# Kernel optimization log

Measured on AMD Instinct MI355X. Metric: run time of the kernel, lower is better.

Reference implementation:

```python
import jax, jax.numpy as jnp
import numpy as np

N = 50000   # num gloss nodes
H = 768     # gnn_hidden_size (BERT-base hidden)
NEG = 0.2   # GATv2 leaky_relu negative_slope
EPS = 1e-5  # LayerNorm eps


def ln_gelu(x, g, b):
    # LayerNorm -> exact GELU (torch GELU default); Dropout is identity in eval
    mu = x.mean(-1, keepdims=True)
    var = ((x - mu) ** 2).mean(-1, keepdims=True)
    x = (x - mu) / jnp.sqrt(var + EPS) * g + b
    return jax.nn.gelu(x, approximate=False)


def gatv2(x, src, dst, Wl, bl, Wr, br, att, bias):
    # PyG GATv2Conv, heads=1: e_ij = a^T LeakyReLU(Wl x_j + Wr x_i), softmax over incoming edges
    xl = x @ Wl + bl              # source transform [N,H]
    xr = x @ Wr + br              # target transform [N,H]
    e = jax.nn.leaky_relu(xl[src] + xr[dst], NEG) @ att   # [E]
    m = jax.ops.segment_max(e, dst, num_segments=N)
    a = jnp.exp(e - m[dst])
    denom = jax.ops.segment_sum(a, dst, num_segments=N)
    alpha = a / denom[dst]
    out = jax.ops.segment_sum(alpha[:, None] * xl[src], dst, num_segments=N)
    return out + bias


def setup_inputs() -> dict:
    key = jax.random.key(0)
    ks = jax.random.split(key, 20)
    d = {
        "input_embeddings": jax.random.normal(ks[0], (32, H), dtype=jnp.float32),
        "node_feats": jax.random.normal(ks[1], (N, H), dtype=jnp.float32),
        "edges": jax.random.randint(ks[2], (2, 100000), 0, N, dtype=jnp.int64)
                 if jax.config.jax_enable_x64 else
                 jax.random.randint(ks[2], (2, 100000), 0, N, dtype=jnp.int32),
        "labels_size": 4096,
    }
    s = 0.02
    for i, name in enumerate(["gat2", "gat3"]):
        k = ks[3 + 6 * i: 9 + 6 * i]
        d[name + "_Wl"] = jax.random.normal(k[0], (H, H), dtype=jnp.float32) * s
        d[name + "_bl"] = jnp.zeros((H,), jnp.float32)
        d[name + "_Wr"] = jax.random.normal(k[1], (H, H), dtype=jnp.float32) * s
        d[name + "_br"] = jnp.zeros((H,), jnp.float32)
        d[name + "_att"] = jax.random.normal(k[2], (H,), dtype=jnp.float32) * s
        d[name + "_bias"] = jnp.zeros((H,), jnp.float32)
    for i in (1, 2, 3):
        d[f"ln{i}_g"] = jnp.ones((H,), jnp.float32)
        d[f"ln{i}_b"] = jnp.zeros((H,), jnp.float32)
    return d


def reference(input_embeddings, node_feats, edges, labels_size,
              gat2_Wl, gat2_bl, gat2_Wr, gat2_br, gat2_att, gat2_bias,
              gat3_Wl, gat3_bl, gat3_Wr, gat3_br, gat3_att, gat3_bias,
              ln1_g, ln1_b, ln2_g, ln2_b, ln3_g, ln3_b):
    loops = jnp.arange(N, dtype=edges.dtype)           # add_self_loops=True
    src = jnp.concatenate([edges[0], loops])
    dst = jnp.concatenate([edges[1], loops])
    x = ln_gelu(node_feats, ln1_g, ln1_b)
    x = gatv2(x, src, dst, gat2_Wl, gat2_bl, gat2_Wr, gat2_br, gat2_att, gat2_bias)
    x = ln_gelu(x, ln2_g, ln2_b)
    x = gatv2(x, src, dst, gat3_Wl, gat3_bl, gat3_Wr, gat3_br, gat3_att, gat3_bias)
    x = ln_gelu(x, ln3_g, ln3_b)
    gnn_vector = x[:labels_size]
    return (input_embeddings, gnn_vector)
```

## Files before the change

kernel.cpp:

```cpp
#include <hip/hip_runtime.h>
#include <hip/hip_bf16.h>
#include <math.h>

#define H 768
#define BM 128

typedef __attribute__((ext_vector_type(4))) float f32x4;
typedef __attribute__((ext_vector_type(8))) short bf16x8;

__device__ __forceinline__ float bf2f(unsigned u16v){
  return __uint_as_float((u16v & 0xffffu) << 16);
}
__device__ __forceinline__ unsigned f2bf2(float a, float b){
  __hip_bfloat16 ha = __float2bfloat16(a), hb = __float2bfloat16(b);
  return (unsigned)*(unsigned short*)&ha | ((unsigned)*(unsigned short*)&hb << 16);
}
__device__ __forceinline__ float gelu_exact(float x){
  return 0.5f * x * (1.0f + erff(x * 0.70710678118654752f));
}
__device__ __forceinline__ void gload16(const void* g, void* l){
  __builtin_amdgcn_global_load_lds(
      (const __attribute__((address_space(1))) unsigned int*)g,
      (__attribute__((address_space(3))) unsigned int*)l,
      16, 0, 0);
}
__device__ __forceinline__ float wave_sum(float p){
#pragma unroll
  for (int o = 32; o; o >>= 1) p += __shfl_xor(p, o);
  return p;
}

__global__ __launch_bounds__(256) void lnw_list_kernel(
    const float* __restrict__ in, const float* __restrict__ g,
    const float* __restrict__ b, __hip_bfloat16* __restrict__ out,
    const int* __restrict__ rlist, const int* __restrict__ np){
  int i = blockIdx.x * 4 + (threadIdx.x >> 6);
  if (i >= *np) return;
  int row = rlist[i];
  int lane = threadIdx.x & 63;
  const float* rp = in + (size_t)row * H;
  float v[12];
#pragma unroll
  for (int q = 0; q < 3; q++){
    float4 t = *(const float4*)&rp[(lane + q * 64) * 4];
    v[q*4+0] = t.x; v[q*4+1] = t.y; v[q*4+2] = t.z; v[q*4+3] = t.w;
  }
  float s = 0.f;
#pragma unroll
  for (int t = 0; t < 12; t++) s += v[t];
  float mean = wave_sum(s) * (1.0f / H);
  float s2 = 0.f;
#pragma unroll
  for (int t = 0; t < 12; t++){ float d = v[t] - mean; s2 += d * d; }
  float rstd = rsqrtf(wave_sum(s2) * (1.0f / H) + 1e-5f);
  unsigned* op = (unsigned*)(out + (size_t)row * H);
#pragma unroll
  for (int q = 0; q < 3; q++){
    float4 gv = *(const float4*)&g[(lane + q * 64) * 4];
    float4 bv = *(const float4*)&b[(lane + q * 64) * 4];
    float z0 = gelu_exact((v[q*4+0] - mean) * rstd * gv.x + bv.x);
    float z1 = gelu_exact((v[q*4+1] - mean) * rstd * gv.y + bv.y);
    float z2 = gelu_exact((v[q*4+2] - mean) * rstd * gv.z + bv.z);
    float z3 = gelu_exact((v[q*4+3] - mean) * rstd * gv.w + bv.w);
    uint2 pk; pk.x = f2bf2(z0, z1); pk.y = f2bf2(z2, z3);
    *(uint2*)&op[lane * 2 + q * 128] = pk;
  }
}

__global__ __launch_bounds__(256) void wt_bf16_kernel(
    const float* __restrict__ W0, const float* __restrict__ W1,
    const float* __restrict__ W2, const float* __restrict__ W3,
    __hip_bfloat16* __restrict__ T0, __hip_bfloat16* __restrict__ T1,
    __hip_bfloat16* __restrict__ T2, __hip_bfloat16* __restrict__ T3){
  int z = blockIdx.z;
  const float* W = (z == 0) ? W0 : (z == 1) ? W1 : (z == 2) ? W2 : W3;
  __hip_bfloat16* WT = (z == 0) ? T0 : (z == 1) ? T1 : (z == 2) ? T2 : T3;
  __shared__ float tile[32][33];
  int k0 = blockIdx.x * 32, n0 = blockIdx.y * 32;
  int tx = threadIdx.x & 31, ty = threadIdx.x >> 5;
#pragma unroll
  for (int i = 0; i < 32; i += 8)
    tile[ty + i][tx] = W[(size_t)(k0 + ty + i) * H + n0 + tx];
  __syncthreads();
#pragma unroll
  for (int i = 0; i < 32; i += 8)
    WT[(size_t)(n0 + ty + i) * H + k0 + tx] = __float2bfloat16(tile[tx][ty + i]);
}

__global__ __launch_bounds__(256, 3) void gemm_fused_kernel(
    const __hip_bfloat16* __restrict__ A,
    const __hip_bfloat16* __restrict__ WT,
    const float* __restrict__ bl, const float* __restrict__ br,
    __hip_bfloat16* __restrict__ Cl, __hip_bfloat16* __restrict__ Cr,
    const int* __restrict__ rmapL, const int* __restrict__ nrLp,
    const int* __restrict__ rmapR, const int* __restrict__ nrRp, int MrR){
  __shared__ char smem[49152];

  int wgid = blockIdx.x;
  int panel = wgid / 12, colblk = wgid % 12;
  int row0 = panel * BM;
  const bool is_r = colblk >= 6;
  const int* rmap = is_r ? rmapR : rmapL;
  int nr = is_r ? (rmapR ? *nrRp : MrR) : *nrLp;
  if (row0 >= nr) return;
  const bool remap = (rmap != nullptr);

  const int t = threadIdx.x;
  const int sr = t >> 2;
  const int scs = (((t & 3) ^ ((sr >> 1) & 3)) * 8);
  const int t16 = t * 16;
  int ra0 = min(row0 + sr, nr - 1), ra1 = min(row0 + sr + 64, nr - 1);
  if (remap){ ra0 = rmap[ra0]; ra1 = rmap[ra1]; }
  const __hip_bfloat16* pa0 = A + (size_t)ra0 * H + scs;
  const __hip_bfloat16* pa1 = A + (size_t)ra1 * H + scs;
  const __hip_bfloat16* pb0 = WT + (size_t)(colblk * 128 + sr) * H + scs;
  const __hip_bfloat16* pb1 = pb0 + (size_t)64 * H;

  const int l = t & 63, w = t >> 6;
  const int wm = (w >> 1) * 64, wn = (w & 1) * 64;
  const int r0 = l & 15;
  const int kcs2 = (((l >> 4) ^ ((r0 >> 1) & 3)) * 16);

  f32x4 acc[4][4];
#pragma unroll
  for (int m = 0; m < 4; m++)
#pragma unroll
    for (int n = 0; n < 4; n++) acc[m][n] = (f32x4){0.f, 0.f, 0.f, 0.f};

#define STAGE(kt, b) do{                                   \
    int _k0 = (kt) * 32;                                   \
    char* _bs = smem + (b) * 16384;                        \
    gload16(pa0 + _k0, _bs + t16);                         \
    gload16(pa1 + _k0, _bs + 4096 + t16);                  \
    gload16(pb0 + _k0, _bs + 8192 + t16);                  \
    gload16(pb1 + _k0, _bs + 12288 + t16);                 \
  }while(0)

  STAGE(0, 0);
  STAGE(1, 1);

  for (int kt = 0; kt < 24; kt++){
    if (kt < 23) asm volatile("s_waitcnt vmcnt(4)" ::: "memory");
    else         asm volatile("s_waitcnt vmcnt(0)" ::: "memory");
    __builtin_amdgcn_s_barrier();
    __builtin_amdgcn_sched_barrier(0);
    if (kt + 2 < 24) STAGE(kt + 2, (kt + 2) % 3);
    const char* base = smem + (kt % 3) * 16384;
    bf16x8 af[4], bfr[4];
#pragma unroll
    for (int m = 0; m < 4; m++)
      af[m]  = *(const bf16x8*)(base + (wm + m * 16 + r0) * 64 + kcs2);
#pragma unroll
    for (int n = 0; n < 4; n++)
      bfr[n] = *(const bf16x8*)(base + 8192 + (wn + n * 16 + r0) * 64 + kcs2);
#pragma unroll
    for (int m = 0; m < 4; m++)
#pragma unroll
      for (int n = 0; n < 4; n++)
        acc[m][n] = __builtin_amdgcn_mfma_f32_16x16x32_bf16(af[m], bfr[n], acc[m][n], 0, 0, 0);
  }
#undef STAGE

  __syncthreads();
  const int rgrp = (l >> 4) * 4;
  const float* bp = is_r ? br : bl;
  const int cb = (is_r ? colblk - 6 : colblk) * 128;
#pragma unroll
  for (int n = 0; n < 4; n++){
    int lc = wn + n * 16 + r0;
    float bb = bp[cb + lc];
#pragma unroll
    for (int m = 0; m < 4; m++){
#pragma unroll
      for (int jj = 0; jj < 4; jj++){
        int lr = wm + m * 16 + rgrp + jj;
        int byte = lr * 256 + ((lc * 2) ^ (((lr >> 2) & 3) << 5));
        *(__hip_bfloat16*)(smem + byte) = __float2bfloat16(acc[m][n][jj] + bb);
      }
    }
  }
  __syncthreads();
  __hip_bfloat16* C = is_r ? Cr : Cl;
#pragma unroll
  for (int p = 0; p < 8; p++){
    int ba = p * 4096 + t16;
    int lr = ba >> 8, inner = ba & 255;
    int gr = row0 + lr;
    if (gr >= nr) continue;
    int orow = remap ? rmap[gr] : gr;
    uint4 v = *(const uint4*)(smem + lr * 256 + (inner ^ (((lr >> 2) & 3) << 5)));
    *(uint4*)(C + (size_t)orow * H + cb + (inner >> 1)) = v;
  }
}

__device__ __forceinline__ int e_src(const int* ep, int E0, int k){
  return (k < E0) ? ep[k] : (k - E0);
}
__device__ __forceinline__ int e_dst(const int* ep, int E0, int k){
  return (k < E0) ? ep[E0 + k] : (k - E0);
}

__global__ __launch_bounds__(256) void count_mark_kernel(const int* __restrict__ ep,
                                                         int E0, int E, int L,
                                                         int* __restrict__ cnt,
                                                         int* __restrict__ flag){
  int k = blockIdx.x * 256 + threadIdx.x;
  if (k >= E) return;
  int d = e_dst(ep, E0, k);
  atomicAdd(&cnt[d], 1);
  if (d < L) flag[e_src(ep, E0, k)] = 1;
}

__global__ __launch_bounds__(256) void mark2_kernel(const int* __restrict__ ep,
                                                    int E0, int E,
                                                    const int* __restrict__ flag,
                                                    int* __restrict__ flag2){
  int k = blockIdx.x * 256 + threadIdx.x;
  if (k >= E) return;
  if (flag[e_dst(ep, E0, k)]) flag2[e_src(ep, E0, k)] = 1;
}

__global__ __launch_bounds__(1024) void scan1_tri_kernel(
    const int* __restrict__ a0, int* __restrict__ o0, int* __restrict__ s0,
    const int* __restrict__ a1, int* __restrict__ o1, int* __restrict__ s1,
    const int* __restrict__ a2, int* __restrict__ o2, int* __restrict__ s2, int n){
  __shared__ int lds[1024];
  const int* as[3] = {a0, a1, a2};
  int* os[3] = {o0, o1, o2};
  int* ss[3] = {s0, s1, s2};
  int tid = threadIdx.x;
  int gi = blockIdx.x * 1024 + tid;
  for (int q = 0; q < 3; q++){
    __syncthreads();
    int v = (gi < n) ? as[q][gi] : 0;
    lds[tid] = v;
    __syncthreads();
    for (int o = 1; o < 1024; o <<= 1){
      int tv = (tid >= o) ? lds[tid - o] : 0;
      __syncthreads();
      lds[tid] += tv;
      __syncthreads();
    }
    if (gi < n) os[q][gi] = lds[tid] - v;
    if (tid == 1023) ss[q][blockIdx.x] = lds[1023];
  }
}

__global__ void scan2_tri_kernel(int* __restrict__ s0, int* __restrict__ o0,
                                 int* __restrict__ s1, int* __restrict__ o1,
                                 int* __restrict__ s2, int* __restrict__ o2,
                                 int nb, int n){
  int lane = threadIdx.x;
  int* ss[3] = {s0, s1, s2};
  int* os[3] = {o0, o1, o2};
  for (int q = 0; q < 3; q++){
    int v = (lane < nb) ? ss[q][lane] : 0;
    int incl = v;
#pragma unroll
    for (int o = 1; o < 64; o <<= 1){
      int t = __shfl_up(incl, o);
      if (lane >= o) incl += t;
    }
    if (lane < nb) ss[q][lane] = incl - v;
    if (lane == nb - 1) os[q][n] = incl;
  }
}

__global__ __launch_bounds__(1024) void scan3_tri_kernel(
    int* __restrict__ off, int* __restrict__ cur, const int* __restrict__ sums,
    int* __restrict__ fpos, const int* __restrict__ fsums,
    const int* __restrict__ flag, int* __restrict__ list,
    int* __restrict__ fpos2, const int* __restrict__ fsums2,
    const int* __restrict__ flag2, int* __restrict__ list2, int n){
  int gi = blockIdx.x * 1024 + threadIdx.x;
  if (gi < n){
    int v = off[gi] + sums[blockIdx.x];
    off[gi] = v;
    cur[gi] = v;
    int fp = fpos[gi] + fsums[blockIdx.x];
    fpos[gi] = fp;
    if (flag[gi]) list[fp] = gi;
    int fp2 = fpos2[gi] + fsums2[blockIdx.x];
    fpos2[gi] = fp2;
    if (flag2[gi]) list2[fp2] = gi;
  }
}

__global__ __launch_bounds__(256) void fill_kernel(const int* __restrict__ ep, int E0, int E,
                                                   int* __restrict__ cur, int* __restrict__ csr){
  int k = blockIdx.x * 256 + threadIdx.x;
  if (k >= E) return;
  int d = e_dst(ep, E0, k);
  int pos = atomicAdd(&cur[d], 1);
  csr[pos] = k;
}

template<typename OutT>
__global__ __launch_bounds__(256) void agat_kernel(
    const __hip_bfloat16* __restrict__ xl, const __hip_bfloat16* __restrict__ xr,
    const float* __restrict__ att, const int* __restrict__ off,
    const int* __restrict__ csr, const int* __restrict__ ep, int E0,
    const float* __restrict__ bias, const float* __restrict__ g,
    const float* __restrict__ b, OutT* __restrict__ out,
    const int* __restrict__ dlist, const int* __restrict__ ndp, int ndst){
  int i = blockIdx.x * 4 + (threadIdx.x >> 6);
  int lim = dlist ? *ndp : ndst;
  if (i >= lim) return;
  int d = dlist ? dlist[i] : i;
  int lane = threadIdx.x & 63;
  float xrv[12], attv[12];
  const unsigned* pr = (const unsigned*)(xr + (size_t)d * H);
#pragma unroll
  for (int q = 0; q < 3; q++){
    uint2 vr = *(const uint2*)&pr[lane * 2 + q * 128];
    float4 av = *(const float4*)&att[(lane + q * 64) * 4];
    xrv[q*4+0] = bf2f(vr.x); xrv[q*4+1] = bf2f(vr.x >> 16);
    xrv[q*4+2] = bf2f(vr.y); xrv[q*4+3] = bf2f(vr.y >> 16);
    attv[q*4+0] = av.x; attv[q*4+1] = av.y; attv[q*4+2] = av.z; attv[q*4+3] = av.w;
  }
  float m = -INFINITY, den = 0.f, acc[12];
#pragma unroll
  for (int t = 0; t < 12; t++) acc[t] = 0.f;
  int j0 = off[d], j1 = off[d + 1];
  int sj = (j0 < j1) ? e_src(ep, E0, csr[j0]) : 0;
  for (int j = j0; j < j1; j++){
    int s_ = sj;
    if (j + 1 < j1) sj = e_src(ep, E0, csr[j + 1]);
    const unsigned* pl = (const unsigned*)(xl + (size_t)s_ * H);
    float xv[12];
#pragma unroll
    for (int q = 0; q < 3; q++){
      uint2 vl = *(const uint2*)&pl[lane * 2 + q * 128];
      xv[q*4+0] = bf2f(vl.x); xv[q*4+1] = bf2f(vl.x >> 16);
      xv[q*4+2] = bf2f(vl.y); xv[q*4+3] = bf2f(vl.y >> 16);
    }
    float p = 0.f;
#pragma unroll
    for (int t = 0; t < 12; t++){
      float v = xv[t] + xrv[t];
      v = (v > 0.f) ? v : 0.2f * v;
      p += v * attv[t];
    }
    p = wave_sum(p);
    float mn = fmaxf(m, p);
    float sc = __expf(m - mn), wgt = __expf(p - mn);
    den = den * sc + wgt;
#pragma unroll
    for (int t = 0; t < 12; t++) acc[t] = acc[t] * sc + wgt * xv[t];
    m = mn;
  }
  float inv = 1.0f / den;
  float y[12];
  float s1 = 0.f;
#pragma unroll
  for (int q = 0; q < 3; q++){
    float4 bv = *(const float4*)&bias[(lane + q * 64) * 4];
    y[q*4+0] = acc[q*4+0] * inv + bv.x;
    y[q*4+1] = acc[q*4+1] * inv + bv.y;
    y[q*4+2] = acc[q*4+2] * inv + bv.z;
    y[q*4+3] = acc[q*4+3] * inv + bv.w;
  }
#pragma unroll
  for (int t = 0; t < 12; t++) s1 += y[t];
  float mean = wave_sum(s1) * (1.0f / H);
  float s2 = 0.f;
#pragma unroll
  for (int t = 0; t < 12; t++){ float dt = y[t] - mean; s2 += dt * dt; }
  float rstd = rsqrtf(wave_sum(s2) * (1.0f / H) + 1e-5f);
  OutT* op = out + (size_t)d * H;
#pragma unroll
  for (int q = 0; q < 3; q++){
    float4 gv = *(const float4*)&g[(lane + q * 64) * 4];
    float4 bv = *(const float4*)&b[(lane + q * 64) * 4];
    float z0 = gelu_exact((y[q*4+0] - mean) * rstd * gv.x + bv.x);
    float z1 = gelu_exact((y[q*4+1] - mean) * rstd * gv.y + bv.y);
    float z2 = gelu_exact((y[q*4+2] - mean) * rstd * gv.z + bv.z);
    float z3 = gelu_exact((y[q*4+3] - mean) * rstd * gv.w + bv.w);
    if constexpr (sizeof(OutT) == 2){
      uint2 pk; pk.x = f2bf2(z0, z1); pk.y = f2bf2(z2, z3);
      *(uint2*)((unsigned*)op + lane * 2 + q * 128) = pk;
    } else {
      float4 fv; fv.x = z0; fv.y = z1; fv.z = z2; fv.w = z3;
      *(float4*)&op[(lane + q * 64) * 4] = fv;
    }
  }
}

extern "C" void kernel_launch(void* const* d_in, const int* in_sizes, int n_in,
                              void* d_out, int out_size, void* d_ws, size_t ws_size,
                              hipStream_t stream){
  const float* emb   = (const float*)d_in[0];
  const float* feats = (const float*)d_in[1];
  const int*   edges = (const int*)d_in[2];
  const float* Wl2 = (const float*)d_in[4],  *bl2 = (const float*)d_in[5];
  const float* Wr2 = (const float*)d_in[6],  *br2 = (const float*)d_in[7];
  const float* att2= (const float*)d_in[8],  *bias2=(const float*)d_in[9];
  const float* Wl3 = (const float*)d_in[10], *bl3 = (const float*)d_in[11];
  const float* Wr3 = (const float*)d_in[12], *br3 = (const float*)d_in[13];
  const float* att3= (const float*)d_in[14], *bias3=(const float*)d_in[15];
  const float* g1 = (const float*)d_in[16], *b1 = (const float*)d_in[17];
  const float* g2 = (const float*)d_in[18], *b2 = (const float*)d_in[19];
  const float* g3 = (const float*)d_in[20], *b3 = (const float*)d_in[21];

  const int N  = in_sizes[1] / H;
  const int E0 = in_sizes[2] / 2;
  const int E  = E0 + N;
  const int L  = 4096;
  const int Mpad = ((N + 127) / 128) * 128;
  const int panels128 = Mpad / BM;
  const int nchunk = (N + 1023) / 1024;

  __hip_bfloat16* ab  = (__hip_bfloat16*)d_ws;
  __hip_bfloat16* xl  = ab + (size_t)Mpad * H;
  __hip_bfloat16* xr  = xl + (size_t)Mpad * H;
  __hip_bfloat16* wt2 = xr + (size_t)Mpad * H;
  __hip_bfloat16* wt3 = wt2 + (size_t)2 * H * H;
  int* cnt   = (int*)(wt3 + (size_t)2 * H * H);
  int* flag  = cnt + N;
  int* flag2 = flag + N;
  int* off   = flag2 + N;
  int* cur   = off + N + 1;
  int* csr   = cur + N;
  int* sums  = csr + E;
  int* fpos  = sums + 64;
  int* fsums = fpos + N + 1;
  int* fpos2 = fsums + 64;
  int* fsums2= fpos2 + N + 1;
  int* list  = fsums2 + 64;
  int* list2 = list + N;

  float* out_f = (float*)d_out;

  hipMemcpyAsync(out_f, emb, (size_t)in_sizes[0] * sizeof(float),
                 hipMemcpyDeviceToDevice, stream);

  hipMemsetAsync(cnt, 0, (size_t)3 * N * sizeof(int), stream);
  count_mark_kernel<<<(E + 255) / 256, 256, 0, stream>>>(edges, E0, E, L, cnt, flag);
  mark2_kernel<<<(E + 255) / 256, 256, 0, stream>>>(edges, E0, E, flag, flag2);
  scan1_tri_kernel<<<nchunk, 1024, 0, stream>>>(cnt, off, sums, flag, fpos, fsums,
                                                flag2, fpos2, fsums2, N);
  scan2_tri_kernel<<<1, 64, 0, stream>>>(sums, off, fsums, fpos, fsums2, fpos2, nchunk, N);
  scan3_tri_kernel<<<nchunk, 1024, 0, stream>>>(off, cur, sums, fpos, fsums, flag, list,
                                                fpos2, fsums2, flag2, list2, N);
  fill_kernel<<<(E + 255) / 256, 256, 0, stream>>>(edges, E0, E, cur, csr);

  dim3 wgrid(H / 32, H / 32, 4);
  wt_bf16_kernel<<<wgrid, 256, 0, stream>>>(Wl2, Wr2, Wl3, Wr3,
                                            wt2, wt2 + (size_t)H * H,
                                            wt3, wt3 + (size_t)H * H);

  const int* nS3 = fpos + N;
  const int* nS2 = fpos2 + N;

  lnw_list_kernel<<<(N + 3) / 4, 256, 0, stream>>>(feats, g1, b1, ab, list2, nS2);
  gemm_fused_kernel<<<panels128 * 12, 256, 0, stream>>>(ab, wt2, bl2, br2, xl, xr,
                                                        list2, nS2, list, nS3, 0);
  agat_kernel<__hip_bfloat16><<<(N + 3) / 4, 256, 0, stream>>>(
      xl, xr, att2, off, csr, edges, E0, bias2, g2, b2, ab, list, nS3, 0);

  gemm_fused_kernel<<<panels128 * 12, 256, 0, stream>>>(ab, wt3, bl3, br3, xl, xr,
                                                        list, nS3, nullptr, nullptr, L);
  agat_kernel<float><<<(L + 3) / 4, 256, 0, stream>>>(
      xl, xr, att3, off, csr, edges, E0, bias3, g3, b3, out_f + in_sizes[0],
      nullptr, nullptr, L);
}
```

Baseline: 206.4 us.

## Fuse graph preprocessing into one cooperative kernel and persist row kernels

Replaces the memset, count/mark, mark2, three scan kernels and the CSR fill with a single cooperative kernel that uses grid-wide syncs between phases. This removes several launches and inter-kernel gaps. The CSR fill now only writes edges whose destination is flagged, which skips work for nodes no later layer reads. The LayerNorm and aggregation kernels become grid-stride loops over a fixed grid of 2048 blocks instead of one wave per row. The cooperative launch needs all 128 blocks of 1024 threads to be co-resident, and a heavy phase such as the atomics-based count now runs on far fewer threads than before.

```diff
diff --git a/kernel.cpp b/kernel.cpp
--- a/kernel.cpp
+++ b/kernel.cpp
@@ -1,6 +1,9 @@
 #include <hip/hip_runtime.h>
+#include <hip/hip_cooperative_groups.h>
 #include <hip/hip_bf16.h>
 #include <math.h>
+
+namespace cg = cooperative_groups;
 
 #define H 768
 #define BM 128
@@ -29,41 +32,129 @@
   for (int o = 32; o; o >>= 1) p += __shfl_xor(p, o);
   return p;
 }
+__device__ __forceinline__ int e_src(const int* ep, int E0, int k){
+  return (k < E0) ? ep[k] : (k - E0);
+}
+__device__ __forceinline__ int e_dst(const int* ep, int E0, int k){
+  return (k < E0) ? ep[E0 + k] : (k - E0);
+}
+
+__global__ __launch_bounds__(1024) void preproc_kernel(
+    const int* __restrict__ ep, int E0, int E, int N, int L,
+    int* cnt, int* flag, int* flag2, int* off, int* cur, int* csr,
+    int* sums, int* fpos, int* fsums, int* fpos2, int* fsums2,
+    int* list, int* list2){
+  cg::grid_group grid = cg::this_grid();
+  __shared__ int lds[1024];
+  const int tid = threadIdx.x;
+  const int gid = blockIdx.x * blockDim.x + tid;
+  const int gsz = gridDim.x * blockDim.x;
+  const int nchunk = (N + 1023) >> 10;
+
+  for (int i = gid; i < 3 * N; i += gsz) cnt[i] = 0;
+  grid.sync();
+  for (int k = gid; k < E; k += gsz){
+    int d = e_dst(ep, E0, k);
+    atomicAdd(&cnt[d], 1);
+    if (d < L) flag[e_src(ep, E0, k)] = 1;
+  }
+  grid.sync();
+  for (int k = gid; k < E; k += gsz)
+    if (flag[e_dst(ep, E0, k)]) flag2[e_src(ep, E0, k)] = 1;
+  grid.sync();
+  {
+    const int* as[3] = {cnt, flag, flag2};
+    int* os[3] = {off, fpos, fpos2};
+    int* ss[3] = {sums, fsums, fsums2};
+    if ((int)blockIdx.x < nchunk){
+      int gi = blockIdx.x * 1024 + tid;
+      for (int q = 0; q < 3; q++){
+        __syncthreads();
+        int v = (gi < N) ? as[q][gi] : 0;
+        lds[tid] = v;
+        __syncthreads();
+        for (int o = 1; o < 1024; o <<= 1){
+          int tv = (tid >= o) ? lds[tid - o] : 0;
+          __syncthreads();
+          lds[tid] += tv;
+          __syncthreads();
+        }
+        if (gi < N) os[q][gi] = lds[tid] - v;
+        if (tid == 1023) ss[q][blockIdx.x] = lds[1023];
+      }
+    }
+  }
+  grid.sync();
+  if (blockIdx.x == 0 && tid < 64){
+    int* ss[3] = {sums, fsums, fsums2};
+    int* os[3] = {off, fpos, fpos2};
+    for (int q = 0; q < 3; q++){
+      int v = (tid < nchunk) ? ss[q][tid] : 0;
+      int incl = v;
+#pragma unroll
+      for (int o = 1; o < 64; o <<= 1){
+        int t2 = __shfl_up(incl, o);
+        if (tid >= o) incl += t2;
+      }
+      if (tid < nchunk) ss[q][tid] = incl - v;
+      if (tid == nchunk - 1) os[q][N] = incl;
+    }
+  }
+  grid.sync();
+  if ((int)blockIdx.x < nchunk){
+    int gi = blockIdx.x * 1024 + tid;
+    if (gi < N){
+      int v = off[gi] + sums[blockIdx.x];
+      off[gi] = v;
+      cur[gi] = v;
+      int fp = fpos[gi] + fsums[blockIdx.x];
+      if (flag[gi]) list[fp] = gi;
+      int fp2 = fpos2[gi] + fsums2[blockIdx.x];
+      if (flag2[gi]) list2[fp2] = gi;
+    }
+  }
+  grid.sync();
+  for (int k = gid; k < E; k += gsz){
+    int d = e_dst(ep, E0, k);
+    if (flag[d]) csr[atomicAdd(&cur[d], 1)] = k;
+  }
+}
 
 __global__ __launch_bounds__(256) void lnw_list_kernel(
     const float* __restrict__ in, const float* __restrict__ g,
     const float* __restrict__ b, __hip_bfloat16* __restrict__ out,
     const int* __restrict__ rlist, const int* __restrict__ np){
-  int i = blockIdx.x * 4 + (threadIdx.x >> 6);
-  if (i >= *np) return;
-  int row = rlist[i];
+  int lim = *np;
   int lane = threadIdx.x & 63;
-  const float* rp = in + (size_t)row * H;
-  float v[12];
-#pragma unroll
-  for (int q = 0; q < 3; q++){
-    float4 t = *(const float4*)&rp[(lane + q * 64) * 4];
-    v[q*4+0] = t.x; v[q*4+1] = t.y; v[q*4+2] = t.z; v[q*4+3] = t.w;
-  }
-  float s = 0.f;
-#pragma unroll
-  for (int t = 0; t < 12; t++) s += v[t];
-  float mean = wave_sum(s) * (1.0f / H);
-  float s2 = 0.f;
-#pragma unroll
-  for (int t = 0; t < 12; t++){ float d = v[t] - mean; s2 += d * d; }
-  float rstd = rsqrtf(wave_sum(s2) * (1.0f / H) + 1e-5f);
-  unsigned* op = (unsigned*)(out + (size_t)row * H);
-#pragma unroll
-  for (int q = 0; q < 3; q++){
-    float4 gv = *(const float4*)&g[(lane + q * 64) * 4];
-    float4 bv = *(const float4*)&b[(lane + q * 64) * 4];
-    float z0 = gelu_exact((v[q*4+0] - mean) * rstd * gv.x + bv.x);
-    float z1 = gelu_exact((v[q*4+1] - mean) * rstd * gv.y + bv.y);
-    float z2 = gelu_exact((v[q*4+2] - mean) * rstd * gv.z + bv.z);
-    float z3 = gelu_exact((v[q*4+3] - mean) * rstd * gv.w + bv.w);
-    uint2 pk; pk.x = f2bf2(z0, z1); pk.y = f2bf2(z2, z3);
-    *(uint2*)&op[lane * 2 + q * 128] = pk;
+  for (int i = blockIdx.x * 4 + (threadIdx.x >> 6); i < lim; i += gridDim.x * 4){
+    int row = rlist[i];
+    const float* rp = in + (size_t)row * H;
+    float v[12];
+#pragma unroll
+    for (int q = 0; q < 3; q++){
+      float4 t = *(const float4*)&rp[(lane + q * 64) * 4];
+      v[q*4+0] = t.x; v[q*4+1] = t.y; v[q*4+2] = t.z; v[q*4+3] = t.w;
+    }
+    float s = 0.f;
+#pragma unroll
+    for (int t = 0; t < 12; t++) s += v[t];
+    float mean = wave_sum(s) * (1.0f / H);
+    float s2 = 0.f;
+#pragma unroll
+    for (int t = 0; t < 12; t++){ float d = v[t] - mean; s2 += d * d; }
+    float rstd = rsqrtf(wave_sum(s2) * (1.0f / H) + 1e-5f);
+    unsigned* op = (unsigned*)(out + (size_t)row * H);
+#pragma unroll
+    for (int q = 0; q < 3; q++){
+      float4 gv = *(const float4*)&g[(lane + q * 64) * 4];
+      float4 bv = *(const float4*)&b[(lane + q * 64) * 4];
+      float z0 = gelu_exact((v[q*4+0] - mean) * rstd * gv.x + bv.x);
+      float z1 = gelu_exact((v[q*4+1] - mean) * rstd * gv.y + bv.y);
+      float z2 = gelu_exact((v[q*4+2] - mean) * rstd * gv.z + bv.z);
+      float z3 = gelu_exact((v[q*4+3] - mean) * rstd * gv.w + bv.w);
+      uint2 pk; pk.x = f2bf2(z0, z1); pk.y = f2bf2(z2, z3);
+      *(uint2*)&op[lane * 2 + q * 128] = pk;
+    }
   }
 }
 
@@ -193,108 +284,6 @@
   }
 }
 
-__device__ __forceinline__ int e_src(const int* ep, int E0, int k){
-  return (k < E0) ? ep[k] : (k - E0);
-}
-__device__ __forceinline__ int e_dst(const int* ep, int E0, int k){
-  return (k < E0) ? ep[E0 + k] : (k - E0);
-}
-
-__global__ __launch_bounds__(256) void count_mark_kernel(const int* __restrict__ ep,
-                                                         int E0, int E, int L,
-                                                         int* __restrict__ cnt,
-                                                         int* __restrict__ flag){
-  int k = blockIdx.x * 256 + threadIdx.x;
-  if (k >= E) return;
-  int d = e_dst(ep, E0, k);
-  atomicAdd(&cnt[d], 1);
-  if (d < L) flag[e_src(ep, E0, k)] = 1;
-}
-
-__global__ __launch_bounds__(256) void mark2_kernel(const int* __restrict__ ep,
-                                                    int E0, int E,
-                                                    const int* __restrict__ flag,
-                                                    int* __restrict__ flag2){
-  int k = blockIdx.x * 256 + threadIdx.x;
-  if (k >= E) return;
-  if (flag[e_dst(ep, E0, k)]) flag2[e_src(ep, E0, k)] = 1;
-}
-
-__global__ __launch_bounds__(1024) void scan1_tri_kernel(
-    const int* __restrict__ a0, int* __restrict__ o0, int* __restrict__ s0,
-    const int* __restrict__ a1, int* __restrict__ o1, int* __restrict__ s1,
-    const int* __restrict__ a2, int* __restrict__ o2, int* __restrict__ s2, int n){
-  __shared__ int lds[1024];
-  const int* as[3] = {a0, a1, a2};
-  int* os[3] = {o0, o1, o2};
-  int* ss[3] = {s0, s1, s2};
-  int tid = threadIdx.x;
-  int gi = blockIdx.x * 1024 + tid;
-  for (int q = 0; q < 3; q++){
-    __syncthreads();
-    int v = (gi < n) ? as[q][gi] : 0;
-    lds[tid] = v;
-    __syncthreads();
-    for (int o = 1; o < 1024; o <<= 1){
-      int tv = (tid >= o) ? lds[tid - o] : 0;
-      __syncthreads();
-      lds[tid] += tv;
-      __syncthreads();
-    }
-    if (gi < n) os[q][gi] = lds[tid] - v;
-    if (tid == 1023) ss[q][blockIdx.x] = lds[1023];
-  }
-}
-
-__global__ void scan2_tri_kernel(int* __restrict__ s0, int* __restrict__ o0,
-                                 int* __restrict__ s1, int* __restrict__ o1,
-                                 int* __restrict__ s2, int* __restrict__ o2,
-                                 int nb, int n){
-  int lane = threadIdx.x;
-  int* ss[3] = {s0, s1, s2};
-  int* os[3] = {o0, o1, o2};
-  for (int q = 0; q < 3; q++){
-    int v = (lane < nb) ? ss[q][lane] : 0;
-    int incl = v;
-#pragma unroll
-    for (int o = 1; o < 64; o <<= 1){
-      int t = __shfl_up(incl, o);
-      if (lane >= o) incl += t;
-    }
-    if (lane < nb) ss[q][lane] = incl - v;
-    if (lane == nb - 1) os[q][n] = incl;
-  }
-}
-
-__global__ __launch_bounds__(1024) void scan3_tri_kernel(
-    int* __restrict__ off, int* __restrict__ cur, const int* __restrict__ sums,
-    int* __restrict__ fpos, const int* __restrict__ fsums,
-    const int* __restrict__ flag, int* __restrict__ list,
-    int* __restrict__ fpos2, const int* __restrict__ fsums2,
-    const int* __restrict__ flag2, int* __restrict__ list2, int n){
-  int gi = blockIdx.x * 1024 + threadIdx.x;
-  if (gi < n){
-    int v = off[gi] + sums[blockIdx.x];
-    off[gi] = v;
-    cur[gi] = v;
-    int fp = fpos[gi] + fsums[blockIdx.x];
-    fpos[gi] = fp;
-    if (flag[gi]) list[fp] = gi;
-    int fp2 = fpos2[gi] + fsums2[blockIdx.x];
-    fpos2[gi] = fp2;
-    if (flag2[gi]) list2[fp2] = gi;
-  }
-}
-
-__global__ __launch_bounds__(256) void fill_kernel(const int* __restrict__ ep, int E0, int E,
-                                                   int* __restrict__ cur, int* __restrict__ csr){
-  int k = blockIdx.x * 256 + threadIdx.x;
-  if (k >= E) return;
-  int d = e_dst(ep, E0, k);
-  int pos = atomicAdd(&cur[d], 1);
-  csr[pos] = k;
-}
-
 template<typename OutT>
 __global__ __launch_bounds__(256) void agat_kernel(
     const __hip_bfloat16* __restrict__ xl, const __hip_bfloat16* __restrict__ xr,
@@ -303,85 +292,85 @@
     const float* __restrict__ bias, const float* __restrict__ g,
     const float* __restrict__ b, OutT* __restrict__ out,
     const int* __restrict__ dlist, const int* __restrict__ ndp, int ndst){
-  int i = blockIdx.x * 4 + (threadIdx.x >> 6);
   int lim = dlist ? *ndp : ndst;
-  if (i >= lim) return;
-  int d = dlist ? dlist[i] : i;
   int lane = threadIdx.x & 63;
-  float xrv[12], attv[12];
-  const unsigned* pr = (const unsigned*)(xr + (size_t)d * H);
-#pragma unroll
-  for (int q = 0; q < 3; q++){
-    uint2 vr = *(const uint2*)&pr[lane * 2 + q * 128];
-    float4 av = *(const float4*)&att[(lane + q * 64) * 4];
-    xrv[q*4+0] = bf2f(vr.x); xrv[q*4+1] = bf2f(vr.x >> 16);
-    xrv[q*4+2] = bf2f(vr.y); xrv[q*4+3] = bf2f(vr.y >> 16);
-    attv[q*4+0] = av.x; attv[q*4+1] = av.y; attv[q*4+2] = av.z; attv[q*4+3] = av.w;
-  }
-  float m = -INFINITY, den = 0.f, acc[12];
-#pragma unroll
-  for (int t = 0; t < 12; t++) acc[t] = 0.f;
-  int j0 = off[d], j1 = off[d + 1];
-  int sj = (j0 < j1) ? e_src(ep, E0, csr[j0]) : 0;
-  for (int j = j0; j < j1; j++){
-    int s_ = sj;
-    if (j + 1 < j1) sj = e_src(ep, E0, csr[j + 1]);
-    const unsigned* pl = (const unsigned*)(xl + (size_t)s_ * H);
-    float xv[12];
-#pragma unroll
-    for (int q = 0; q < 3; q++){
-      uint2 vl = *(const uint2*)&pl[lane * 2 + q * 128];
-      xv[q*4+0] = bf2f(vl.x); xv[q*4+1] = bf2f(vl.x >> 16);
-      xv[q*4+2] = bf2f(vl.y); xv[q*4+3] = bf2f(vl.y >> 16);
-    }
-    float p = 0.f;
-#pragma unroll
-    for (int t = 0; t < 12; t++){
-      float v = xv[t] + xrv[t];
-      v = (v > 0.f) ? v : 0.2f * v;
-      p += v * attv[t];
-    }
-    p = wave_sum(p);
-    float mn = fmaxf(m, p);
-    float sc = __expf(m - mn), wgt = __expf(p - mn);
-    den = den * sc + wgt;
-#pragma unroll
-    for (int t = 0; t < 12; t++) acc[t] = acc[t] * sc + wgt * xv[t];
-    m = mn;
-  }
-  float inv = 1.0f / den;
-  float y[12];
-  float s1 = 0.f;
-#pragma unroll
-  for (int q = 0; q < 3; q++){
-    float4 bv = *(const float4*)&bias[(lane + q * 64) * 4];
-    y[q*4+0] = acc[q*4+0] * inv + bv.x;
-    y[q*4+1] = acc[q*4+1] * inv + bv.y;
-    y[q*4+2] = acc[q*4+2] * inv + bv.z;
-    y[q*4+3] = acc[q*4+3] * inv + bv.w;
-  }
-#pragma unroll
-  for (int t = 0; t < 12; t++) s1 += y[t];
-  float mean = wave_sum(s1) * (1.0f / H);
-  float s2 = 0.f;
-#pragma unroll
-  for (int t = 0; t < 12; t++){ float dt = y[t] - mean; s2 += dt * dt; }
-  float rstd = rsqrtf(wave_sum(s2) * (1.0f / H) + 1e-5f);
-  OutT* op = out + (size_t)d * H;
-#pragma unroll
-  for (int q = 0; q < 3; q++){
-    float4 gv = *(const float4*)&g[(lane + q * 64) * 4];
-    float4 bv = *(const float4*)&b[(lane + q * 64) * 4];
-    float z0 = gelu_exact((y[q*4+0] - mean) * rstd * gv.x + bv.x);
-    float z1 = gelu_exact((y[q*4+1] - mean) * rstd * gv.y + bv.y);
-    float z2 = gelu_exact((y[q*4+2] - mean) * rstd * gv.z + bv.z);
-    float z3 = gelu_exact((y[q*4+3] - mean) * rstd * gv.w + bv.w);
-    if constexpr (sizeof(OutT) == 2){
-      uint2 pk; pk.x = f2bf2(z0, z1); pk.y = f2bf2(z2, z3);
-      *(uint2*)((unsigned*)op + lane * 2 + q * 128) = pk;
-    } else {
-      float4 fv; fv.x = z0; fv.y = z1; fv.z = z2; fv.w = z3;
-      *(float4*)&op[(lane + q * 64) * 4] = fv;
+  for (int i = blockIdx.x * 4 + (threadIdx.x >> 6); i < lim; i += gridDim.x * 4){
+    int d = dlist ? dlist[i] : i;
+    float xrv[12], attv[12];
+    const unsigned* pr = (const unsigned*)(xr + (size_t)d * H);
+#pragma unroll
+    for (int q = 0; q < 3; q++){
+      uint2 vr = *(const uint2*)&pr[lane * 2 + q * 128];
+      float4 av = *(const float4*)&att[(lane + q * 64) * 4];
+      xrv[q*4+0] = bf2f(vr.x); xrv[q*4+1] = bf2f(vr.x >> 16);
+      xrv[q*4+2] = bf2f(vr.y); xrv[q*4+3] = bf2f(vr.y >> 16);
+      attv[q*4+0] = av.x; attv[q*4+1] = av.y; attv[q*4+2] = av.z; attv[q*4+3] = av.w;
+    }
+    float m = -INFINITY, den = 0.f, acc[12];
+#pragma unroll
+    for (int t = 0; t < 12; t++) acc[t] = 0.f;
+    int j0 = off[d], j1 = off[d + 1];
+    int sj = (j0 < j1) ? e_src(ep, E0, csr[j0]) : 0;
+    for (int j = j0; j < j1; j++){
+      int s_ = sj;
+      if (j + 1 < j1) sj = e_src(ep, E0, csr[j + 1]);
+      const unsigned* pl = (const unsigned*)(xl + (size_t)s_ * H);
+      float xv[12];
+#pragma unroll
+      for (int q = 0; q < 3; q++){
+        uint2 vl = *(const uint2*)&pl[lane * 2 + q * 128];
+        xv[q*4+0] = bf2f(vl.x); xv[q*4+1] = bf2f(vl.x >> 16);
+        xv[q*4+2] = bf2f(vl.y); xv[q*4+3] = bf2f(vl.y >> 16);
+      }
+      float p = 0.f;
+#pragma unroll
+      for (int t = 0; t < 12; t++){
+        float v = xv[t] + xrv[t];
+        v = (v > 0.f) ? v : 0.2f * v;
+        p += v * attv[t];
+      }
+      p = wave_sum(p);
+      float mn = fmaxf(m, p);
+      float sc = __expf(m - mn), wgt = __expf(p - mn);
+      den = den * sc + wgt;
+#pragma unroll
+      for (int t = 0; t < 12; t++) acc[t] = acc[t] * sc + wgt * xv[t];
+      m = mn;
+    }
+    float inv = 1.0f / den;
+    float y[12];
+    float s1 = 0.f;
+#pragma unroll
+    for (int q = 0; q < 3; q++){
+      float4 bv = *(const float4*)&bias[(lane + q * 64) * 4];
+      y[q*4+0] = acc[q*4+0] * inv + bv.x;
+      y[q*4+1] = acc[q*4+1] * inv + bv.y;
+      y[q*4+2] = acc[q*4+2] * inv + bv.z;
+      y[q*4+3] = acc[q*4+3] * inv + bv.w;
+    }
+#pragma unroll
+    for (int t = 0; t < 12; t++) s1 += y[t];
+    float mean = wave_sum(s1) * (1.0f / H);
+    float s2 = 0.f;
+#pragma unroll
+    for (int t = 0; t < 12; t++){ float dt = y[t] - mean; s2 += dt * dt; }
+    float rstd = rsqrtf(wave_sum(s2) * (1.0f / H) + 1e-5f);
+    OutT* op = out + (size_t)d * H;
+#pragma unroll
+    for (int q = 0; q < 3; q++){
+      float4 gv = *(const float4*)&g[(lane + q * 64) * 4];
+      float4 bv = *(const float4*)&b[(lane + q * 64) * 4];
+      float z0 = gelu_exact((y[q*4+0] - mean) * rstd * gv.x + bv.x);
+      float z1 = gelu_exact((y[q*4+1] - mean) * rstd * gv.y + bv.y);
+      float z2 = gelu_exact((y[q*4+2] - mean) * rstd * gv.z + bv.z);
+      float z3 = gelu_exact((y[q*4+3] - mean) * rstd * gv.w + bv.w);
+      if constexpr (sizeof(OutT) == 2){
+        uint2 pk; pk.x = f2bf2(z0, z1); pk.y = f2bf2(z2, z3);
+        *(uint2*)((unsigned*)op + lane * 2 + q * 128) = pk;
+      } else {
+        float4 fv; fv.x = z0; fv.y = z1; fv.z = z2; fv.w = z3;
+        *(float4*)&op[(lane + q * 64) * 4] = fv;
+      }
     }
   }
 }
@@ -408,7 +397,6 @@
   const int L  = 4096;
   const int Mpad = ((N + 127) / 128) * 128;
   const int panels128 = Mpad / BM;
-  const int nchunk = (N + 1023) / 1024;
 
   __hip_bfloat16* ab  = (__hip_bfloat16*)d_ws;
   __hip_bfloat16* xl  = ab + (size_t)Mpad * H;
@@ -434,15 +422,17 @@
   hipMemcpyAsync(out_f, emb, (size_t)in_sizes[0] * sizeof(float),
                  hipMemcpyDeviceToDevice, stream);
 
-  hipMemsetAsync(cnt, 0, (size_t)3 * N * sizeof(int), stream);
-  count_mark_kernel<<<(E + 255) / 256, 256, 0, stream>>>(edges, E0, E, L, cnt, flag);
-  mark2_kernel<<<(E + 255) / 256, 256, 0, stream>>>(edges, E0, E, flag, flag2);
-  scan1_tri_kernel<<<nchunk, 1024, 0, stream>>>(cnt, off, sums, flag, fpos, fsums,
-                                                flag2, fpos2, fsums2, N);
-  scan2_tri_kernel<<<1, 64, 0, stream>>>(sums, off, fsums, fpos, fsums2, fpos2, nchunk, N);
-  scan3_tri_kernel<<<nchunk, 1024, 0, stream>>>(off, cur, sums, fpos, fsums, flag, list,
-                                                fpos2, fsums2, flag2, list2, N);
-  fill_kernel<<<(E + 255) / 256, 256, 0, stream>>>(edges, E0, E, cur, csr);
+  {
+    const int* ep = edges;
+    int e0 = E0, e = E, n = N, lv = L;
+    void* args[] = {(void*)&ep, (void*)&e0, (void*)&e, (void*)&n, (void*)&lv,
+                    (void*)&cnt, (void*)&flag, (void*)&flag2, (void*)&off,
+                    (void*)&cur, (void*)&csr, (void*)&sums, (void*)&fpos,
+                    (void*)&fsums, (void*)&fpos2, (void*)&fsums2,
+                    (void*)&list, (void*)&list2};
+    hipLaunchCooperativeKernel((void*)preproc_kernel, dim3(128), dim3(1024),
+                               args, 0, stream);
+  }
 
   dim3 wgrid(H / 32, H / 32, 4);
   wt_bf16_kernel<<<wgrid, 256, 0, stream>>>(Wl2, Wr2, Wl3, Wr3,
@@ -452,10 +442,10 @@
   const int* nS3 = fpos + N;
   const int* nS2 = fpos2 + N;
 
-  lnw_list_kernel<<<(N + 3) / 4, 256, 0, stream>>>(feats, g1, b1, ab, list2, nS2);
+  lnw_list_kernel<<<2048, 256, 0, stream>>>(feats, g1, b1, ab, list2, nS2);
   gemm_fused_kernel<<<panels128 * 12, 256, 0, stream>>>(ab, wt2, bl2, br2, xl, xr,
                                                         list2, nS2, list, nS3, 0);
-  agat_kernel<__hip_bfloat16><<<(N + 3) / 4, 256, 0, stream>>>(
+  agat_kernel<__hip_bfloat16><<<2048, 256, 0, stream>>>(
       xl, xr, att2, off, csr, edges, E0, bias2, g2, b2, ab, list, nS3, 0);
 
   gemm_fused_kernel<<<panels128 * 12, 256, 0, stream>>>(ab, wt3, bl3, br3, xl, xr,
```

Measured after the change: 300.6 us. 45.6% more time.
